# Kernel optimization log

Hardware: AMD Instinct MI355X
Metric: run time of the kernel (lower is better)

The kernel has to match this reference:

```python
import jax, jax.numpy as jnp
import numpy as np

N, E, IN_DIM, HID, HEADS, L, G, NODES_PER_G = 131072, 524288, 78, 64, 4, 3, 4096, 32
NEG_SLOPE = 0.2


def setup_inputs() -> dict:
    key = jax.random.key(0)
    ks = jax.random.split(key, 20)
    inp = {
        "x": jax.random.normal(ks[0], (N, IN_DIM), jnp.float32),
        "edge_index": jax.random.randint(ks[1], (2, E), 0, N, jnp.int32),
        "batch": (jnp.arange(N, dtype=jnp.int32) // NODES_PER_G),
    }
    dims = [IN_DIM, HID, HID]
    for l in range(L):
        d_in = dims[l]
        inp[f"W{l}"] = jax.random.normal(ks[2 + 4 * l], (d_in, HEADS * HID), jnp.float32) / np.sqrt(d_in)
        inp[f"a_src{l}"] = jax.random.normal(ks[3 + 4 * l], (HEADS, HID), jnp.float32) / np.sqrt(HID)
        inp[f"a_dst{l}"] = jax.random.normal(ks[4 + 4 * l], (HEADS, HID), jnp.float32) / np.sqrt(HID)
        inp[f"b{l}"] = jnp.zeros((HID,), jnp.float32)
    inp["pw"] = jax.random.normal(ks[14], (HID, 1), jnp.float32) / np.sqrt(HID)
    inp["pb"] = jnp.zeros((1,), jnp.float32)
    return inp


def _gat_layer(x, W, a_src, a_dst, b, src, dst):
    # PyG GATConv, concat=False: mean over heads, bias after aggregation.
    h = (x @ W).reshape(N, HEADS, HID)                      # [N,H,D]
    alpha_s = jnp.einsum("nhd,hd->nh", h, a_src)            # [N,H]
    alpha_d = jnp.einsum("nhd,hd->nh", h, a_dst)
    e = jax.nn.leaky_relu(alpha_s[src] + alpha_d[dst], NEG_SLOPE)  # [E',H]
    # scatter-softmax over edges grouped by destination node
    m = jax.ops.segment_max(e, dst, num_segments=N)
    e = jnp.exp(e - m[dst])
    denom = jax.ops.segment_sum(e, dst, num_segments=N)
    alpha = e / denom[dst]                                   # self-loops => denom > 0
    msg = h[src] * alpha[..., None]                          # [E',H,D]
    out = jax.ops.segment_sum(msg, dst, num_segments=N)      # [N,H,D]
    return out.mean(axis=1) + b                              # [N,D]


def reference(x, edge_index, batch, W0, a_src0, a_dst0, b0, W1, a_src1, a_dst1, b1,
              W2, a_src2, a_dst2, b2, pw, pb):
    loop = jnp.arange(N, dtype=edge_index.dtype)
    src = jnp.concatenate([edge_index[0], loop])             # add self loops (PyG default)
    dst = jnp.concatenate([edge_index[1], loop])
    params = [(W0, a_src0, a_dst0, b0), (W1, a_src1, a_dst1, b1), (W2, a_src2, a_dst2, b2)]
    pooled = []
    h = x
    for (W, asr, ads, b) in params:
        h = jax.nn.relu(_gat_layer(h, W, asr, ads, b, src, dst))
        pooled.append(jax.ops.segment_sum(h, batch, num_segments=G))  # global_add_pool
    hstack = jnp.stack(pooled, axis=1)                       # [G,L,D]
    logits = (hstack @ pw).squeeze(-1) + pb                  # [G,L]
    attn = jax.nn.softmax(logits, axis=1)
    return jnp.einsum("gld,gl->gd", hstack, attn)            # [G,D]
```

## Files before the change

### kernel.cpp

```cpp
#include <hip/hip_runtime.h>
#include <math.h>

#define N_NODES 131072
#define N_EDGES 524288
#define IN_DIM_ 78
#define HID_ 64
#define HEADS_ 4
#define NG 4096
#define NPG 32
#define NLAYERS 3
#define NEG_SLOPE 0.2f

typedef __attribute__((ext_vector_type(8))) short bf16x8;
typedef __attribute__((ext_vector_type(4))) float f32x4;

__device__ __forceinline__ unsigned short f2bf(float f) {
    unsigned int u = __float_as_uint(f);
    u = (u + 0x7FFF + ((u >> 16) & 1)) >> 16;
    return (unsigned short)u;
}
__device__ __forceinline__ float bf2f(unsigned short u) {
    return __uint_as_float(((unsigned int)u) << 16);
}


__global__ void init_counts(int* __restrict__ cnt) {
    int n = blockIdx.x * blockDim.x + threadIdx.x;
    if (n < N_NODES) cnt[n] = 1;
}

__global__ void count_edges(const int* __restrict__ dst, int* __restrict__ cnt) {
    int e = blockIdx.x * blockDim.x + threadIdx.x;
    if (e < N_EDGES) atomicAdd(&cnt[dst[e]], 1);
}

__global__ void scan_kernel(const int* __restrict__ cnt, int* __restrict__ offsets) {
    __shared__ int sums[1024];
    const int t = threadIdx.x;
    const int CHUNK = N_NODES / 1024;
    int base = t * CHUNK;
    int s = 0;
    for (int j = 0; j < CHUNK / 4; ++j) {
        int4 v = ((const int4*)(cnt + base))[j];
        s += v.x + v.y + v.z + v.w;
    }
    sums[t] = s;
    __syncthreads();
    for (int off = 1; off < 1024; off <<= 1) {
        int v = (t >= off) ? sums[t - off] : 0;
        __syncthreads();
        sums[t] += v;
        __syncthreads();
    }
    int run = (t == 0) ? 0 : sums[t - 1];
    for (int j = 0; j < CHUNK / 4; ++j) {
        int4 c = ((const int4*)(cnt + base))[j];
        int4 o;
        o.x = run; run += c.x;
        o.y = run; run += c.y;
        o.z = run; run += c.z;
        o.w = run; run += c.w;
        ((int4*)(offsets + base))[j] = o;
    }
    if (t == 1023) offsets[N_NODES] = run;
}

__global__ void place_self(const int* __restrict__ offsets, int* __restrict__ cursor,
                           int* __restrict__ csr_src) {
    int n = blockIdx.x * blockDim.x + threadIdx.x;
    if (n < N_NODES) {
        int o = offsets[n];
        csr_src[o] = n;
        cursor[n] = o + 1;
    }
}

__global__ void scatter_edges(const int* __restrict__ src, const int* __restrict__ dst,
                              int* __restrict__ cursor, int* __restrict__ csr_src) {
    int e = blockIdx.x * blockDim.x + threadIdx.x;
    if (e < N_EDGES) {
        int d = dst[e];
        int pos = atomicAdd(&cursor[d], 1);
        csr_src[pos] = src[e];
    }
}

__global__ void wsplit_frag(const float* __restrict__ W, int K,
                            unsigned short* __restrict__ WfH, unsigned short* __restrict__ WfL) {
    int idx = blockIdx.x * 256 + threadIdx.x;
    int k = idx >> 8, col = idx & 255;
    float w = (k < K) ? W[k * 256 + col] : 0.f;
    unsigned short hi = f2bf(w);
    unsigned short lo = f2bf(w - bf2f(hi));
    int ch = k >> 5, kk = k & 31;
    int lg = kk >> 3, j = kk & 7;
    int ct = col >> 4, li = col & 15;
    size_t o = (((size_t)ch * 18 + ct) * 64 + (lg * 16 + li)) * 8 + j;
    WfH[o] = hi;
    WfL[o] = lo;
}

__global__ void waug(const float* __restrict__ W, const float* __restrict__ asrc,
                     const float* __restrict__ adst, int K,
                     unsigned short* __restrict__ WfH, unsigned short* __restrict__ WfL) {
    int k = blockIdx.x;
    int t = threadIdx.x;
    int tile = 16 + (t >> 4), li = t & 15;
    float v = 0.f;
    if (li < 4 && k < K) {
        const float* a = (tile == 16) ? asrc : adst;
        const float* wr = W + k * 256 + li * 64;
        #pragma unroll 8
        for (int d = 0; d < 64; ++d) v += wr[d] * a[li * 64 + d];
    }
    unsigned short hi = f2bf(v);
    unsigned short lo = f2bf(v - bf2f(hi));
    int ch = k >> 5, kk = k & 31;
    int lg = kk >> 3, j = kk & 7;
    size_t o = (((size_t)ch * 18 + tile) * 64 + (lg * 16 + li)) * 8 + j;
    WfH[o] = hi;
    WfL[o] = lo;
}

template<int NCH, int K>
__global__ __launch_bounds__(256)
void gemm_mfma(const float* __restrict__ A,
               const unsigned short* __restrict__ WfH,
               const unsigned short* __restrict__ WfL,
               unsigned short* __restrict__ h, float* __restrict__ als, float* __restrict__ ald) {
    const int tid = threadIdx.x;
    const int w = tid >> 6;
    const int lane = tid & 63;
    const int li = lane & 15, lg = lane >> 4;
    const int row0 = blockIdx.x * 64;
    const int r0 = (w >> 1) * 32;
    const int cw = w & 1;

    bf16x8 ah[NCH][2], al[NCH][2];
    #pragma unroll
    for (int ch = 0; ch < NCH; ++ch) {
        #pragma unroll
        for (int rt = 0; rt < 2; ++rt) {
            const int row = row0 + r0 + rt * 16 + li;
            const int kb = ch * 32 + lg * 8;
            float t[8];
            if ((ch + 1) * 32 <= K) {
                if constexpr ((K % 4) == 0) {
                    const float4* ap = (const float4*)(A + (size_t)row * K + kb);
                    float4 v0 = ap[0], v1 = ap[1];
                    t[0] = v0.x; t[1] = v0.y; t[2] = v0.z; t[3] = v0.w;
                    t[4] = v1.x; t[5] = v1.y; t[6] = v1.z; t[7] = v1.w;
                } else {
                    const float2* ap = (const float2*)(A + (size_t)row * K + kb);
                    #pragma unroll
                    for (int j = 0; j < 4; ++j) {
                        float2 v = ap[j];
                        t[2 * j] = v.x; t[2 * j + 1] = v.y;
                    }
                }
            } else {
                const float2* ap = (const float2*)(A + (size_t)row * K + kb);
                #pragma unroll
                for (int j = 0; j < 4; ++j) {
                    float2 v = (kb + 2 * j + 1 < K) ? ap[j] : make_float2(0.f, 0.f);
                    t[2 * j] = v.x; t[2 * j + 1] = v.y;
                }
            }
            bf16x8 hh, ll;
            #pragma unroll
            for (int j = 0; j < 8; ++j) {
                unsigned short hi = f2bf(t[j]);
                unsigned short lo = f2bf(t[j] - bf2f(hi));
                hh[j] = (short)hi; ll[j] = (short)lo;
            }
            ah[ch][rt] = hh; al[ch][rt] = ll;
        }
    }

    f32x4 acc[2][9];
    #pragma unroll
    for (int rt = 0; rt < 2; ++rt)
        #pragma unroll
        for (int ci = 0; ci < 9; ++ci)
            acc[rt][ci] = (f32x4){0.f, 0.f, 0.f, 0.f};

    #pragma unroll
    for (int ch = 0; ch < NCH; ++ch) {
        #pragma unroll
        for (int ci = 0; ci < 9; ++ci) {
            const int t = (ci < 8) ? (cw * 8 + ci) : (16 + cw);
            const size_t fo = (((size_t)ch * 18 + t) * 64 + lane) * 8;
            bf16x8 bh = *(const bf16x8*)&WfH[fo];
            bf16x8 bl = *(const bf16x8*)&WfL[fo];
            acc[0][ci] = __builtin_amdgcn_mfma_f32_16x16x32_bf16(ah[ch][0], bh, acc[0][ci], 0, 0, 0);
            acc[1][ci] = __builtin_amdgcn_mfma_f32_16x16x32_bf16(ah[ch][1], bh, acc[1][ci], 0, 0, 0);
            acc[0][ci] = __builtin_amdgcn_mfma_f32_16x16x32_bf16(al[ch][0], bh, acc[0][ci], 0, 0, 0);
            acc[1][ci] = __builtin_amdgcn_mfma_f32_16x16x32_bf16(al[ch][1], bh, acc[1][ci], 0, 0, 0);
            acc[0][ci] = __builtin_amdgcn_mfma_f32_16x16x32_bf16(ah[ch][0], bl, acc[0][ci], 0, 0, 0);
            acc[1][ci] = __builtin_amdgcn_mfma_f32_16x16x32_bf16(ah[ch][1], bl, acc[1][ci], 0, 0, 0);
        }
    }

    #pragma unroll
    for (int rt = 0; rt < 2; ++rt) {
        #pragma unroll
        for (int ci = 0; ci < 8; ++ci) {
            #pragma unroll
            for (int reg = 0; reg < 4; ++reg) {
                int row = row0 + r0 + rt * 16 + lg * 4 + reg;
                int col = cw * 128 + ci * 16 + li;
                h[(size_t)row * 256 + col] = f2bf(acc[rt][ci][reg]);
            }
        }
    }
    float* __restrict__ tgt = cw ? ald : als;
    #pragma unroll
    for (int rt = 0; rt < 2; ++rt) {
        #pragma unroll
        for (int reg = 0; reg < 4; ++reg) {
            int row = row0 + r0 + rt * 16 + lg * 4 + reg;
            if (li < 4) tgt[row * 4 + li] = acc[rt][8][reg];
        }
    }
}

__device__ __forceinline__ float pick4(float4 v, int idx) {
    float r = v.x;
    r = (idx == 1) ? v.y : r;
    r = (idx == 2) ? v.z : r;
    r = (idx == 3) ? v.w : r;
    return r;
}

__global__ __launch_bounds__(256)
void aggregate(const int* __restrict__ offsets, const int* __restrict__ csr_src,
               const unsigned short* __restrict__ h, const float* __restrict__ als,
               const float* __restrict__ ald, const float* __restrict__ bias,
               float* __restrict__ hout) {
    const int lane = threadIdx.x & 63;
    const int wid = __builtin_amdgcn_readfirstlane(threadIdx.x >> 6);
    const int n = blockIdx.x * 4 + wid;
    const int head = lane >> 4;
    const int d4 = (lane & 15) * 4;

    const int o0 = __builtin_amdgcn_readfirstlane(offsets[n]);
    const int o1 = __builtin_amdgcn_readfirstlane(offsets[n + 1]);

    const float ad_h = pick4(*(const float4*)&ald[n * 4], head);

    float4 acc = make_float4(0.f, 0.f, 0.f, 0.f);
    float den = 0.f;

    int i = o0;
    for (; i + 4 <= o1; i += 4) {
        int s0 = __builtin_amdgcn_readfirstlane(csr_src[i + 0]);
        int s1 = __builtin_amdgcn_readfirstlane(csr_src[i + 1]);
        int s2 = __builtin_amdgcn_readfirstlane(csr_src[i + 2]);
        int s3 = __builtin_amdgcn_readfirstlane(csr_src[i + 3]);
        float4 as0 = *(const float4*)&als[s0 * 4];
        float4 as1 = *(const float4*)&als[s1 * 4];
        float4 as2 = *(const float4*)&als[s2 * 4];
        float4 as3 = *(const float4*)&als[s3 * 4];
        ushort4 u0 = ((const ushort4*)(h + (size_t)s0 * 256))[lane];
        ushort4 u1 = ((const ushort4*)(h + (size_t)s1 * 256))[lane];
        ushort4 u2 = ((const ushort4*)(h + (size_t)s2 * 256))[lane];
        ushort4 u3 = ((const ushort4*)(h + (size_t)s3 * 256))[lane];
        float e0 = pick4(as0, head) + ad_h; e0 = e0 > 0.f ? e0 : NEG_SLOPE * e0;
        float e1 = pick4(as1, head) + ad_h; e1 = e1 > 0.f ? e1 : NEG_SLOPE * e1;
        float e2 = pick4(as2, head) + ad_h; e2 = e2 > 0.f ? e2 : NEG_SLOPE * e2;
        float e3 = pick4(as3, head) + ad_h; e3 = e3 > 0.f ? e3 : NEG_SLOPE * e3;
        float p0 = __expf(e0), p1 = __expf(e1), p2 = __expf(e2), p3 = __expf(e3);
        den += p0 + p1 + p2 + p3;
        acc.x += p0 * bf2f(u0.x) + p1 * bf2f(u1.x) + p2 * bf2f(u2.x) + p3 * bf2f(u3.x);
        acc.y += p0 * bf2f(u0.y) + p1 * bf2f(u1.y) + p2 * bf2f(u2.y) + p3 * bf2f(u3.y);
        acc.z += p0 * bf2f(u0.z) + p1 * bf2f(u1.z) + p2 * bf2f(u2.z) + p3 * bf2f(u3.z);
        acc.w += p0 * bf2f(u0.w) + p1 * bf2f(u1.w) + p2 * bf2f(u2.w) + p3 * bf2f(u3.w);
    }
    for (; i < o1; ++i) {
        int s = __builtin_amdgcn_readfirstlane(csr_src[i]);
        float4 asv = *(const float4*)&als[s * 4];
        ushort4 uv = ((const ushort4*)(h + (size_t)s * 256))[lane];
        float e = pick4(asv, head) + ad_h;
        e = e > 0.f ? e : NEG_SLOPE * e;
        float p = __expf(e);
        den += p;
        acc.x += p * bf2f(uv.x); acc.y += p * bf2f(uv.y);
        acc.z += p * bf2f(uv.z); acc.w += p * bf2f(uv.w);
    }

    const float rden = 1.f / den;
    float c0 = acc.x * rden, c1 = acc.y * rden, c2 = acc.z * rden, c3 = acc.w * rden;
    c0 += __shfl_xor(c0, 16, 64); c0 += __shfl_xor(c0, 32, 64);
    c1 += __shfl_xor(c1, 16, 64); c1 += __shfl_xor(c1, 32, 64);
    c2 += __shfl_xor(c2, 16, 64); c2 += __shfl_xor(c2, 32, 64);
    c3 += __shfl_xor(c3, 16, 64); c3 += __shfl_xor(c3, 32, 64);

    if (lane < 16) {
        float4 bv = *(const float4*)&bias[d4];
        float v0 = 0.25f * c0 + bv.x;
        float v1 = 0.25f * c1 + bv.y;
        float v2 = 0.25f * c2 + bv.z;
        float v3 = 0.25f * c3 + bv.w;
        float4 o;
        o.x = v0 > 0.f ? v0 : 0.f;
        o.y = v1 > 0.f ? v1 : 0.f;
        o.z = v2 > 0.f ? v2 : 0.f;
        o.w = v3 > 0.f ? v3 : 0.f;
        *(float4*)&hout[(size_t)n * 64 + d4] = o;
    }
}

__global__ __launch_bounds__(256)
void pool_kernel(const float* __restrict__ hout, float* __restrict__ pooled, int layer) {
    const int wid = threadIdx.x >> 6, lane = threadIdx.x & 63;
    const int g = blockIdx.x * 4 + wid;
    float s = 0.f;
    const float* p = &hout[(size_t)g * NPG * 64 + lane];
    #pragma unroll 8
    for (int i = 0; i < NPG; ++i) s += p[i * 64];
    pooled[(g * NLAYERS + layer) * 64 + lane] = s;
}

__global__ __launch_bounds__(256)
void final_kernel(const float* __restrict__ pooled, const float* __restrict__ pw,
                  const float* __restrict__ pb, float* __restrict__ out) {
    const int wid = threadIdx.x >> 6, lane = threadIdx.x & 63;
    const int g = blockIdx.x * 4 + wid;
    float v0 = pooled[(g * 3 + 0) * 64 + lane];
    float v1 = pooled[(g * 3 + 1) * 64 + lane];
    float v2 = pooled[(g * 3 + 2) * 64 + lane];
    float w = pw[lane];
    float l0 = v0 * w, l1 = v1 * w, l2 = v2 * w;
    #pragma unroll
    for (int m = 1; m < 64; m <<= 1) {
        l0 += __shfl_xor(l0, m, 64);
        l1 += __shfl_xor(l1, m, 64);
        l2 += __shfl_xor(l2, m, 64);
    }
    float bb = pb[0];
    l0 += bb; l1 += bb; l2 += bb;
    float mx = fmaxf(l0, fmaxf(l1, l2));
    float e0 = __expf(l0 - mx), e1 = __expf(l1 - mx), e2 = __expf(l2 - mx);
    float inv = 1.f / (e0 + e1 + e2);
    out[(size_t)g * 64 + lane] = (v0 * e0 + v1 * e1 + v2 * e2) * inv;
}

extern "C" void kernel_launch(void* const* d_in, const int* in_sizes, int n_in,
                              void* d_out, int out_size, void* d_ws, size_t ws_size,
                              hipStream_t stream) {
    const float* x  = (const float*)d_in[0];
    const int*   ei = (const int*)d_in[1];
    const float* W[3]    = {(const float*)d_in[3], (const float*)d_in[7],  (const float*)d_in[11]};
    const float* asrc[3] = {(const float*)d_in[4], (const float*)d_in[8],  (const float*)d_in[12]};
    const float* adst[3] = {(const float*)d_in[5], (const float*)d_in[9],  (const float*)d_in[13]};
    const float* bias[3] = {(const float*)d_in[6], (const float*)d_in[10], (const float*)d_in[14]};
    const float* pw = (const float*)d_in[15];
    const float* pb = (const float*)d_in[16];
    float* out = (float*)d_out;

    char* ws = (char*)d_ws;
    size_t off = 0;
    auto alloc = [&](size_t bytes) -> void* {
        void* p = ws + off;
        off = (off + bytes + 255) & ~(size_t)255;
        return p;
    };
    int*   offsets = (int*)alloc((N_NODES + 1) * 4);
    int*   cursor  = (int*)alloc(N_NODES * 4);
    int*   csr_src = (int*)alloc((size_t)(N_EDGES + N_NODES) * 4);
    unsigned short* h = (unsigned short*)alloc((size_t)N_NODES * 256 * 2);
    float* als     = (float*)alloc((size_t)N_NODES * 4 * 4);
    float* ald     = (float*)alloc((size_t)N_NODES * 4 * 4);
    float* hbuf0   = (float*)alloc((size_t)N_NODES * 64 * 4);
    float* hbuf1   = (float*)alloc((size_t)N_NODES * 64 * 4);
    float* pooled  = (float*)alloc((size_t)NG * 3 * 64 * 4);
    unsigned short* WfH = (unsigned short*)alloc((size_t)3 * 18 * 64 * 8 * 2);
    unsigned short* WfL = (unsigned short*)alloc((size_t)3 * 18 * 64 * 8 * 2);
    (void)ws_size; (void)in_sizes; (void)n_in; (void)out_size;

    const int* srcp = ei;
    const int* dstp = ei + N_EDGES;

    init_counts<<<N_NODES / 256, 256, 0, stream>>>(cursor);
    count_edges<<<N_EDGES / 256, 256, 0, stream>>>(dstp, cursor);
    scan_kernel<<<1, 1024, 0, stream>>>(cursor, offsets);
    place_self<<<N_NODES / 256, 256, 0, stream>>>(offsets, cursor, csr_src);
    scatter_edges<<<N_EDGES / 256, 256, 0, stream>>>(srcp, dstp, cursor, csr_src);

    const float* in = x;
    for (int l = 0; l < 3; ++l) {
        const int K = (l == 0) ? IN_DIM_ : HID_;
        wsplit_frag<<<96, 256, 0, stream>>>(W[l], K, WfH, WfL);
        waug<<<96, 32, 0, stream>>>(W[l], asrc[l], adst[l], K, WfH, WfL);
        if (l == 0)
            gemm_mfma<3, IN_DIM_><<<N_NODES / 64, 256, 0, stream>>>(in, WfH, WfL, h, als, ald);
        else
            gemm_mfma<2, HID_><<<N_NODES / 64, 256, 0, stream>>>(in, WfH, WfL, h, als, ald);
        float* ho = (l & 1) ? hbuf1 : hbuf0;
        aggregate<<<N_NODES / 4, 256, 0, stream>>>(offsets, csr_src, h, als, ald, bias[l], ho);
        pool_kernel<<<NG / 4, 256, 0, stream>>>(ho, pooled, l);
        in = ho;
    }
    final_kernel<<<NG / 4, 256, 0, stream>>>(pooled, pw, pb, out);
}
```

Before: 535.2 us.

## Parallelize CSR scan, batch weight prep, fuse pooling into aggregate via atomics

Replaces the single-block 1024-thread scan with a three-kernel multi-block scan and folds the self-loop placement into the final scan pass. The per-layer weight split and augmentation kernels are merged into one launch that prepares all three layers up front. The separate pooling kernel is removed: aggregate now atomically adds each node's output into the pooled buffer, which init_counts zeroes. Fewer and shorter launches come at the cost of many float atomics, which also makes the pooled sums order-dependent.

```diff
diff --git a/kernel.cpp b/kernel.cpp
--- a/kernel.cpp
+++ b/kernel.cpp
@@ -10,6 +10,8 @@
 #define NPG 32
 #define NLAYERS 3
 #define NEG_SLOPE 0.2f
+#define SCAN_BLOCKS 128
+#define WF_LSTRIDE 27648
 
 typedef __attribute__((ext_vector_type(8))) short bf16x8;
 typedef __attribute__((ext_vector_type(4))) float f32x4;
@@ -24,9 +26,10 @@
 }
 
 
-__global__ void init_counts(int* __restrict__ cnt) {
+__global__ void init_counts(int* __restrict__ cnt, float* __restrict__ pooled) {
     int n = blockIdx.x * blockDim.x + threadIdx.x;
     if (n < N_NODES) cnt[n] = 1;
+    for (int j = n; j < NG * NLAYERS * 64; j += N_NODES) pooled[j] = 0.f;
 }
 
 __global__ void count_edges(const int* __restrict__ dst, int* __restrict__ cnt) {
@@ -34,45 +37,58 @@
     if (e < N_EDGES) atomicAdd(&cnt[dst[e]], 1);
 }
 
-__global__ void scan_kernel(const int* __restrict__ cnt, int* __restrict__ offsets) {
-    __shared__ int sums[1024];
-    const int t = threadIdx.x;
-    const int CHUNK = N_NODES / 1024;
-    int base = t * CHUNK;
-    int s = 0;
-    for (int j = 0; j < CHUNK / 4; ++j) {
-        int4 v = ((const int4*)(cnt + base))[j];
-        s += v.x + v.y + v.z + v.w;
-    }
-    sums[t] = s;
+__global__ void blocksum(const int* __restrict__ cnt, int* __restrict__ part) {
+    __shared__ int red[4];
+    int b = blockIdx.x, t = threadIdx.x;
+    int4 v = ((const int4*)cnt)[b * 256 + t];
+    int s = v.x + v.y + v.z + v.w;
+    #pragma unroll
+    for (int m = 1; m < 64; m <<= 1) s += __shfl_xor(s, m, 64);
+    if ((t & 63) == 0) red[t >> 6] = s;
     __syncthreads();
-    for (int off = 1; off < 1024; off <<= 1) {
-        int v = (t >= off) ? sums[t - off] : 0;
+    if (t == 0) part[b] = red[0] + red[1] + red[2] + red[3];
+}
+
+__global__ void scanpart(int* __restrict__ part) {
+    __shared__ int sh[SCAN_BLOCKS];
+    int t = threadIdx.x;
+    int v = part[t];
+    sh[t] = v;
+    __syncthreads();
+    for (int off = 1; off < SCAN_BLOCKS; off <<= 1) {
+        int u = (t >= off) ? sh[t - off] : 0;
         __syncthreads();
-        sums[t] += v;
+        sh[t] += u;
         __syncthreads();
     }
-    int run = (t == 0) ? 0 : sums[t - 1];
-    for (int j = 0; j < CHUNK / 4; ++j) {
-        int4 c = ((const int4*)(cnt + base))[j];
-        int4 o;
-        o.x = run; run += c.x;
-        o.y = run; run += c.y;
-        o.z = run; run += c.z;
-        o.w = run; run += c.w;
-        ((int4*)(offsets + base))[j] = o;
-    }
-    if (t == 1023) offsets[N_NODES] = run;
-}
-
-__global__ void place_self(const int* __restrict__ offsets, int* __restrict__ cursor,
-                           int* __restrict__ csr_src) {
-    int n = blockIdx.x * blockDim.x + threadIdx.x;
-    if (n < N_NODES) {
-        int o = offsets[n];
-        csr_src[o] = n;
-        cursor[n] = o + 1;
-    }
+    part[t] = sh[t] - v;
+}
+
+__global__ void scanfinal(const int* __restrict__ cnt, const int* __restrict__ part,
+                          int* __restrict__ offsets, int* __restrict__ cursor,
+                          int* __restrict__ csr_src) {
+    __shared__ int sh[256];
+    int b = blockIdx.x, t = threadIdx.x;
+    int idx4 = b * 256 + t;
+    int4 c = ((const int4*)cnt)[idx4];
+    int ts = c.x + c.y + c.z + c.w;
+    sh[t] = ts;
+    __syncthreads();
+    for (int off = 1; off < 256; off <<= 1) {
+        int u = (t >= off) ? sh[t - off] : 0;
+        __syncthreads();
+        sh[t] += u;
+        __syncthreads();
+    }
+    int run = part[b] + sh[t] - ts;
+    int n = idx4 * 4;
+    int4 o;
+    o.x = run; csr_src[run] = n;     cursor[n]     = run + 1; run += c.x;
+    o.y = run; csr_src[run] = n + 1; cursor[n + 1] = run + 1; run += c.y;
+    o.z = run; csr_src[run] = n + 2; cursor[n + 2] = run + 1; run += c.z;
+    o.w = run; csr_src[run] = n + 3; cursor[n + 3] = run + 1; run += c.w;
+    ((int4*)offsets)[idx4] = o;
+    if (b == SCAN_BLOCKS - 1 && t == 255) offsets[N_NODES] = run;
 }
 
 __global__ void scatter_edges(const int* __restrict__ src, const int* __restrict__ dst,
@@ -85,41 +101,48 @@
     }
 }
 
-__global__ void wsplit_frag(const float* __restrict__ W, int K,
-                            unsigned short* __restrict__ WfH, unsigned short* __restrict__ WfL) {
-    int idx = blockIdx.x * 256 + threadIdx.x;
-    int k = idx >> 8, col = idx & 255;
-    float w = (k < K) ? W[k * 256 + col] : 0.f;
-    unsigned short hi = f2bf(w);
-    unsigned short lo = f2bf(w - bf2f(hi));
-    int ch = k >> 5, kk = k & 31;
-    int lg = kk >> 3, j = kk & 7;
-    int ct = col >> 4, li = col & 15;
-    size_t o = (((size_t)ch * 18 + ct) * 64 + (lg * 16 + li)) * 8 + j;
-    WfH[o] = hi;
-    WfL[o] = lo;
-}
-
-__global__ void waug(const float* __restrict__ W, const float* __restrict__ asrc,
-                     const float* __restrict__ adst, int K,
-                     unsigned short* __restrict__ WfH, unsigned short* __restrict__ WfL) {
-    int k = blockIdx.x;
-    int t = threadIdx.x;
-    int tile = 16 + (t >> 4), li = t & 15;
-    float v = 0.f;
-    if (li < 4 && k < K) {
-        const float* a = (tile == 16) ? asrc : adst;
-        const float* wr = W + k * 256 + li * 64;
-        #pragma unroll 8
-        for (int d = 0; d < 64; ++d) v += wr[d] * a[li * 64 + d];
-    }
-    unsigned short hi = f2bf(v);
-    unsigned short lo = f2bf(v - bf2f(hi));
-    int ch = k >> 5, kk = k & 31;
-    int lg = kk >> 3, j = kk & 7;
-    size_t o = (((size_t)ch * 18 + tile) * 64 + (lg * 16 + li)) * 8 + j;
-    WfH[o] = hi;
-    WfL[o] = lo;
+__global__ void wprep(const float* __restrict__ W0, const float* __restrict__ W1,
+                      const float* __restrict__ W2,
+                      const float* __restrict__ as0, const float* __restrict__ as1,
+                      const float* __restrict__ as2,
+                      const float* __restrict__ ad0, const float* __restrict__ ad1,
+                      const float* __restrict__ ad2,
+                      unsigned short* __restrict__ WfH, unsigned short* __restrict__ WfL) {
+    int b = blockIdx.x;
+    int l = b / 96, k = b - l * 96;
+    const float* W    = (l == 0) ? W0  : (l == 1) ? W1  : W2;
+    const float* asrc = (l == 0) ? as0 : (l == 1) ? as1 : as2;
+    const float* adst = (l == 0) ? ad0 : (l == 1) ? ad1 : ad2;
+    const int K = (l == 0) ? IN_DIM_ : HID_;
+    const size_t base = (size_t)l * WF_LSTRIDE;
+    const int ch = k >> 5, kk = k & 31;
+    const int lg = kk >> 3, j = kk & 7;
+
+    int col = threadIdx.x;
+    {
+        float w = (k < K) ? W[k * 256 + col] : 0.f;
+        unsigned short hi = f2bf(w);
+        unsigned short lo = f2bf(w - bf2f(hi));
+        int ct = col >> 4, li = col & 15;
+        size_t o = base + (((size_t)ch * 18 + ct) * 64 + (lg * 16 + li)) * 8 + j;
+        WfH[o] = hi;
+        WfL[o] = lo;
+    }
+    if (col < 32) {
+        int tile = 16 + (col >> 4), li = col & 15;
+        float v = 0.f;
+        if (li < 4 && k < K) {
+            const float* a = (tile == 16) ? asrc : adst;
+            const float* wr = W + k * 256 + li * 64;
+            #pragma unroll 8
+            for (int d = 0; d < 64; ++d) v += wr[d] * a[li * 64 + d];
+        }
+        unsigned short hi = f2bf(v);
+        unsigned short lo = f2bf(v - bf2f(hi));
+        size_t o = base + (((size_t)ch * 18 + tile) * 64 + (lg * 16 + li)) * 8 + j;
+        WfH[o] = hi;
+        WfL[o] = lo;
+    }
 }
 
 template<int NCH, int K>
@@ -236,7 +259,7 @@
 void aggregate(const int* __restrict__ offsets, const int* __restrict__ csr_src,
                const unsigned short* __restrict__ h, const float* __restrict__ als,
                const float* __restrict__ ald, const float* __restrict__ bias,
-               float* __restrict__ hout) {
+               float* __restrict__ hout, float* __restrict__ pooled, int layer) {
     const int lane = threadIdx.x & 63;
     const int wid = __builtin_amdgcn_readfirstlane(threadIdx.x >> 6);
     const int n = blockIdx.x * 4 + wid;
@@ -261,10 +284,10 @@
         float4 as1 = *(const float4*)&als[s1 * 4];
         float4 as2 = *(const float4*)&als[s2 * 4];
         float4 as3 = *(const float4*)&als[s3 * 4];
-        ushort4 u0 = ((const ushort4*)(h + (size_t)s0 * 256))[lane];
-        ushort4 u1 = ((const ushort4*)(h + (size_t)s1 * 256))[lane];
-        ushort4 u2 = ((const ushort4*)(h + (size_t)s2 * 256))[lane];
-        ushort4 u3 = ((const ushort4*)(h + (size_t)s3 * 256))[lane];
+        ushort4 u0 = ((const ushort4*)h)[(unsigned)(s0 * 64 + lane)];
+        ushort4 u1 = ((const ushort4*)h)[(unsigned)(s1 * 64 + lane)];
+        ushort4 u2 = ((const ushort4*)h)[(unsigned)(s2 * 64 + lane)];
+        ushort4 u3 = ((const ushort4*)h)[(unsigned)(s3 * 64 + lane)];
         float e0 = pick4(as0, head) + ad_h; e0 = e0 > 0.f ? e0 : NEG_SLOPE * e0;
         float e1 = pick4(as1, head) + ad_h; e1 = e1 > 0.f ? e1 : NEG_SLOPE * e1;
         float e2 = pick4(as2, head) + ad_h; e2 = e2 > 0.f ? e2 : NEG_SLOPE * e2;
@@ -279,7 +302,7 @@
     for (; i < o1; ++i) {
         int s = __builtin_amdgcn_readfirstlane(csr_src[i]);
         float4 asv = *(const float4*)&als[s * 4];
-        ushort4 uv = ((const ushort4*)(h + (size_t)s * 256))[lane];
+        ushort4 uv = ((const ushort4*)h)[(unsigned)(s * 64 + lane)];
         float e = pick4(asv, head) + ad_h;
         e = e > 0.f ? e : NEG_SLOPE * e;
         float p = __expf(e);
@@ -307,18 +330,12 @@
         o.z = v2 > 0.f ? v2 : 0.f;
         o.w = v3 > 0.f ? v3 : 0.f;
         *(float4*)&hout[(size_t)n * 64 + d4] = o;
-    }
-}
-
-__global__ __launch_bounds__(256)
-void pool_kernel(const float* __restrict__ hout, float* __restrict__ pooled, int layer) {
-    const int wid = threadIdx.x >> 6, lane = threadIdx.x & 63;
-    const int g = blockIdx.x * 4 + wid;
-    float s = 0.f;
-    const float* p = &hout[(size_t)g * NPG * 64 + lane];
-    #pragma unroll 8
-    for (int i = 0; i < NPG; ++i) s += p[i * 64];
-    pooled[(g * NLAYERS + layer) * 64 + lane] = s;
+        float* pp = &pooled[((n >> 5) * NLAYERS + layer) * 64 + d4];
+        atomicAdd(pp + 0, o.x);
+        atomicAdd(pp + 1, o.y);
+        atomicAdd(pp + 2, o.z);
+        atomicAdd(pp + 3, o.w);
+    }
 }
 
 __global__ __launch_bounds__(256)
@@ -368,37 +385,41 @@
     int*   offsets = (int*)alloc((N_NODES + 1) * 4);
     int*   cursor  = (int*)alloc(N_NODES * 4);
     int*   csr_src = (int*)alloc((size_t)(N_EDGES + N_NODES) * 4);
+    int*   part    = (int*)alloc(SCAN_BLOCKS * 4);
     unsigned short* h = (unsigned short*)alloc((size_t)N_NODES * 256 * 2);
     float* als     = (float*)alloc((size_t)N_NODES * 4 * 4);
     float* ald     = (float*)alloc((size_t)N_NODES * 4 * 4);
     float* hbuf0   = (float*)alloc((size_t)N_NODES * 64 * 4);
     float* hbuf1   = (float*)alloc((size_t)N_NODES * 64 * 4);
-    float* pooled  = (float*)alloc((size_t)NG * 3 * 64 * 4);
-    unsigned short* WfH = (unsigned short*)alloc((size_t)3 * 18 * 64 * 8 * 2);
-    unsigned short* WfL = (unsigned short*)alloc((size_t)3 * 18 * 64 * 8 * 2);
+    float* pooled  = (float*)alloc((size_t)NG * NLAYERS * 64 * 4);
+    unsigned short* WfH = (unsigned short*)alloc((size_t)NLAYERS * WF_LSTRIDE * 2);
+    unsigned short* WfL = (unsigned short*)alloc((size_t)NLAYERS * WF_LSTRIDE * 2);
     (void)ws_size; (void)in_sizes; (void)n_in; (void)out_size;
 
     const int* srcp = ei;
     const int* dstp = ei + N_EDGES;
 
-    init_counts<<<N_NODES / 256, 256, 0, stream>>>(cursor);
+    init_counts<<<N_NODES / 256, 256, 0, stream>>>(cursor, pooled);
     count_edges<<<N_EDGES / 256, 256, 0, stream>>>(dstp, cursor);
-    scan_kernel<<<1, 1024, 0, stream>>>(cursor, offsets);
-    place_self<<<N_NODES / 256, 256, 0, stream>>>(offsets, cursor, csr_src);
+    blocksum<<<SCAN_BLOCKS, 256, 0, stream>>>(cursor, part);
+    scanpart<<<1, SCAN_BLOCKS, 0, stream>>>(part);
+    scanfinal<<<SCAN_BLOCKS, 256, 0, stream>>>(cursor, part, offsets, cursor, csr_src);
     scatter_edges<<<N_EDGES / 256, 256, 0, stream>>>(srcp, dstp, cursor, csr_src);
+    wprep<<<NLAYERS * 96, 256, 0, stream>>>(W[0], W[1], W[2],
+                                            asrc[0], asrc[1], asrc[2],
+                                            adst[0], adst[1], adst[2], WfH, WfL);
 
     const float* in = x;
     for (int l = 0; l < 3; ++l) {
-        const int K = (l == 0) ? IN_DIM_ : HID_;
-        wsplit_frag<<<96, 256, 0, stream>>>(W[l], K, WfH, WfL);
-        waug<<<96, 32, 0, stream>>>(W[l], asrc[l], adst[l], K, WfH, WfL);
+        const unsigned short* wfh = WfH + (size_t)l * WF_LSTRIDE;
+        const unsigned short* wfl = WfL + (size_t)l * WF_LSTRIDE;
         if (l == 0)
-            gemm_mfma<3, IN_DIM_><<<N_NODES / 64, 256, 0, stream>>>(in, WfH, WfL, h, als, ald);
+            gemm_mfma<3, IN_DIM_><<<N_NODES / 64, 256, 0, stream>>>(in, wfh, wfl, h, als, ald);
         else
-            gemm_mfma<2, HID_><<<N_NODES / 64, 256, 0, stream>>>(in, WfH, WfL, h, als, ald);
+            gemm_mfma<2, HID_><<<N_NODES / 64, 256, 0, stream>>>(in, wfh, wfl, h, als, ald);
         float* ho = (l & 1) ? hbuf1 : hbuf0;
-        aggregate<<<N_NODES / 4, 256, 0, stream>>>(offsets, csr_src, h, als, ald, bias[l], ho);
-        pool_kernel<<<NG / 4, 256, 0, stream>>>(ho, pooled, l);
+        aggregate<<<N_NODES / 4, 256, 0, stream>>>(offsets, csr_src, h, als, ald, bias[l],
+                                                   ho, pooled, l);
         in = ho;
     }
     final_kernel<<<NG / 4, 256, 0, stream>>>(pooled, pw, pb, out);
```

New measurement: 924.5 us. 1.73x slower.
